# Performance work log

Measured on AMD Instinct MI355X. Metric: run time of the kernel, lower is better.

Reference implementation:

```python
import jax, jax.numpy as jnp
import numpy as np

N = 200000   # active voxels
B = 2        # batch size
G = 128      # spatial grid extent per axis
CIN = 64
COUT = 64
KS = 3       # kernel size -> 27 offsets
DIL = 1
EPS = 1e-5


def setup_inputs() -> dict:
    rng = np.random.default_rng(0)
    # unique active voxel coordinates over a B x G^3 grid
    lin = rng.choice(B * G * G * G, size=N, replace=False)
    b = lin // (G * G * G)
    r = lin % (G * G * G)
    x = r // (G * G)
    r2 = r % (G * G)
    y = r2 // G
    z = r2 % G
    coords = jnp.asarray(np.stack([b, x, y, z], axis=1).astype(np.int32))
    key = jax.random.key(0)
    ks = jax.random.split(key, 7)
    feats = jax.random.normal(ks[0], (N, CIN), jnp.float32)
    s1 = 1.0 / np.sqrt(KS ** 3 * CIN)
    s2 = 1.0 / np.sqrt(KS ** 3 * COUT)
    return {
        "feats": feats,
        "w1": jax.random.normal(ks[1], (KS ** 3, CIN, COUT), jnp.float32) * s1,
        "g1": 1.0 + 0.1 * jax.random.normal(ks[2], (COUT,), jnp.float32),
        "b1": 0.1 * jax.random.normal(ks[3], (COUT,), jnp.float32),
        "w2": jax.random.normal(ks[4], (KS ** 3, COUT, COUT), jnp.float32) * s2,
        "g2": 1.0 + 0.1 * jax.random.normal(ks[5], (COUT,), jnp.float32),
        "b2": 0.1 * jax.random.normal(ks[6], (COUT,), jnp.float32),
        "coords": coords,
    }


def build_neighbors(coords):
    """Hash (dense) lookup: for each of 27 kernel offsets, the input index of
    the neighboring active voxel (submanifold: output sites == input sites).
    Returns idx [27, N] int32 (0 where invalid) and mask [27, N] bool."""
    n = coords.shape[0]
    lin = ((coords[:, 0] * G + coords[:, 1]) * G + coords[:, 2]) * G + coords[:, 3]
    table = jnp.full((B * G * G * G,), -1, jnp.int32).at[lin].set(
        jnp.arange(n, dtype=jnp.int32))
    offs = jnp.asarray(
        [[dx, dy, dz] for dx in (-1, 0, 1) for dy in (-1, 0, 1) for dz in (-1, 0, 1)],
        dtype=jnp.int32) * DIL                       # [27, 3]
    nxyz = coords[None, :, 1:] + offs[:, None, :]    # [27, N, 3]
    inb = jnp.all((nxyz >= 0) & (nxyz < G), axis=-1)  # [27, N]
    c = jnp.clip(nxyz, 0, G - 1)
    nlin = ((coords[None, :, 0] * G + c[..., 0]) * G + c[..., 1]) * G + c[..., 2]
    idx = table[nlin]                                # [27, N]
    mask = inb & (idx >= 0)
    return jnp.where(mask, idx, 0), mask


def subm_conv(feats, nbr_idx, nbr_mask, w):
    # gather-GEMM-scatter, accumulated per kernel offset
    out = jnp.zeros((feats.shape[0], w.shape[-1]), feats.dtype)
    for k in range(w.shape[0]):
        g = jnp.where(nbr_mask[k][:, None], feats[nbr_idx[k]], 0.0)  # [N, Cin]
        out = out + g @ w[k]
    return out


def sparse_bn(x, gamma, beta):
    m = jnp.mean(x, axis=0)
    v = jnp.var(x, axis=0)
    return (x - m) * jax.lax.rsqrt(v + EPS) * gamma + beta


def reference(feats, w1, g1, b1, w2, g2, b2, coords):
    nbr_idx, nbr_mask = build_neighbors(coords)
    h = jax.nn.relu(sparse_bn(subm_conv(feats, nbr_idx, nbr_mask, w1), g1, b1))
    h = sparse_bn(subm_conv(h, nbr_idx, nbr_mask, w2), g2, b2)
    # shortcut is Identity (in_channels == out_channels, stride == 1)
    return jax.nn.relu(h + feats)
```

## Files before the change

kernel.cpp:

```cpp
#include <hip/hip_runtime.h>


constexpr int N_VOX = 200000;
constexpr int GEXT  = 128;
constexpr int C     = 64;
constexpr int K27   = 27;
constexpr int TBL_N = 2 * GEXT * GEXT * GEXT;
constexpr float EPSF = 1e-5f;

constexpr int NCH      = 782;
constexpr int PAIR_CAP = 460032;
constexpr int TIL64    = PAIR_CAP / 64;
constexpr int PBB      = 6250;
constexpr int RBLK     = 128;
constexpr int PAIRS_BLKS = K27 * NCH;
constexpr int PREP_FEAT  = 12500;
constexpr int PREP_W     = 432;

using short8   = __attribute__((ext_vector_type(8))) short;
using floatx16 = __attribute__((ext_vector_type(16))) float;

static __device__ __forceinline__ ushort f2bf(float f) {
  union { float f; unsigned u; } a; a.f = f;
  unsigned r = a.u + 0x7fff + ((a.u >> 16) & 1);
  return (ushort)(r >> 16);
}
static __device__ __forceinline__ float bf2f(ushort h) {
  union { unsigned u; float f; } a; a.u = ((unsigned)h) << 16;
  return a.f;
}


__global__ __launch_bounds__(256) void k_fill(int* __restrict__ t,
                                              int* __restrict__ bsum) {
  int i = blockIdx.x * 256 + threadIdx.x;
  if (i < TBL_N) t[i] = -1;
  if (i < 4096) bsum[i] = 0;
}

__global__ __launch_bounds__(256) void k_scatcnt(const int* __restrict__ coords,
                                                 int* __restrict__ t,
                                                 int* __restrict__ bsum) {
  int n = blockIdx.x * 256 + threadIdx.x;
  if (n >= N_VOX) return;
  int4 c = reinterpret_cast<const int4*>(coords)[n];
  int lin = ((c.x * GEXT + c.y) * GEXT + c.z) * GEXT + c.w;
  t[lin] = n;
  atomicAdd(&bsum[lin >> 10], 1);
}

__global__ __launch_bounds__(1024) void k_scan(const int* __restrict__ bsum,
                                               int* __restrict__ boff) {
  __shared__ int sc[1024];
  int t = threadIdx.x;
  int v0 = bsum[t * 4], v1 = bsum[t * 4 + 1], v2 = bsum[t * 4 + 2],
      v3 = bsum[t * 4 + 3];
  int s = v0 + v1 + v2 + v3;
  sc[t] = s;
  __syncthreads();
  for (int off = 1; off < 1024; off <<= 1) {
    int x = (t >= off) ? sc[t - off] : 0;
    __syncthreads();
    sc[t] += x;
    __syncthreads();
  }
  int excl = sc[t] - s;
  boff[t * 4]     = excl;
  boff[t * 4 + 1] = excl + v0;
  boff[t * 4 + 2] = excl + v0 + v1;
  boff[t * 4 + 3] = excl + v0 + v1 + v2;
}

__global__ __launch_bounds__(1024) void k_compact(int* __restrict__ table,
                                                  const int* __restrict__ boff,
                                                  int* __restrict__ perm) {
  __shared__ int wsum[16];
  int i = blockIdx.x * 1024 + threadIdx.x;
  int orig = table[i];
  bool valid = orig >= 0;
  unsigned long long bal = __ballot(valid);
  int lane = threadIdx.x & 63, wv = threadIdx.x >> 6;
  int before = __popcll(bal & ((1ull << lane) - 1ull));
  if (lane == 0) wsum[wv] = __popcll(bal);
  __syncthreads();
  int woff = 0;
  for (int w = 0; w < 16; ++w) woff += (w < wv) ? wsum[w] : 0;
  if (valid) {
    int j = boff[blockIdx.x] + woff + before;
    perm[j] = orig;
    table[i] = j;
  }
}

__global__ __launch_bounds__(256) void k_nbrc(const int* __restrict__ coords,
                                              const int* __restrict__ table,
                                              const int* __restrict__ perm,
                                              int* __restrict__ nbrp,
                                              int* __restrict__ cnt2,
                                              unsigned* __restrict__ vmask) {
  __shared__ int wcnt[27][4];
  int tid = threadIdx.x;
  int j = blockIdx.x * 256 + tid;
  bool on = j < N_VOX;
  int4 c = {0, 0, 0, 0};
  if (on) {
    int orig = perm[j];
    c = reinterpret_cast<const int4*>(coords)[orig];
  }
  unsigned m = 0;
  int k = 0;
  #pragma unroll
  for (int dx = -1; dx <= 1; ++dx)
    #pragma unroll
    for (int dy = -1; dy <= 1; ++dy)
      #pragma unroll
      for (int dz = -1; dz <= 1; ++dz) {
        int rank = -1;
        if (on) {
          int x = c.y + dx, y = c.z + dy, z = c.w + dz;
          if (((unsigned)x < (unsigned)GEXT) & ((unsigned)y < (unsigned)GEXT) &
              ((unsigned)z < (unsigned)GEXT)) {
            int lin = ((c.x * GEXT + x) * GEXT + y) * GEXT + z;
            rank = table[lin];
          }
          nbrp[k * N_VOX + j] = rank;
          if (rank >= 0) m |= (1u << k);
        }
        unsigned long long bal = __ballot(rank >= 0);
        if ((tid & 63) == 0) wcnt[k][tid >> 6] = __popcll(bal);
        ++k;
      }
  if (on) vmask[j] = m;
  __syncthreads();
  if (tid < 27)
    cnt2[tid * NCH + blockIdx.x] =
        wcnt[tid][0] + wcnt[tid][1] + wcnt[tid][2] + wcnt[tid][3];
}

__global__ __launch_bounds__(256) void k_segscan(const int* __restrict__ cnt2,
                                                 int* __restrict__ choff,
                                                 int* __restrict__ segs) {
  __shared__ int sc[256];
  int k = blockIdx.x, t = threadIdx.x;
  int v[4];
  #pragma unroll
  for (int i = 0; i < 4; ++i) {
    int idx = t * 4 + i;
    v[i] = (idx < NCH) ? cnt2[k * NCH + idx] : 0;
  }
  int s = v[0] + v[1] + v[2] + v[3];
  sc[t] = s;
  __syncthreads();
  for (int off = 1; off < 256; off <<= 1) {
    int x = (t >= off) ? sc[t - off] : 0;
    __syncthreads();
    sc[t] += x;
    __syncthreads();
  }
  int run = sc[t] - s;
  #pragma unroll
  for (int i = 0; i < 4; ++i) {
    int idx = t * 4 + i;
    if (idx < NCH) choff[k * NCH + idx] = run;
    run += v[i];
  }
  if (t == 255) segs[k] = sc[255];
}

__global__ __launch_bounds__(1024) void k_tiles(int* __restrict__ segs,
                                                int* __restrict__ tilk) {
  __shared__ int sb[28];
  if (threadIdx.x == 0) {
    int b = 0;
    for (int k = 0; k < K27; ++k) {
      sb[k] = b;
      segs[32 + k] = b;
      b += (segs[k] + 63) & ~63;
    }
    sb[27] = b;
    segs[32 + K27] = b;
  }
  __syncthreads();
  for (int t = threadIdx.x; t < TIL64; t += 1024) {
    int p0 = t * 64, kk = -1;
    #pragma unroll 1
    for (int k = 0; k < K27; ++k)
      if (p0 >= sb[k] && p0 < sb[k + 1]) kk = k;
    tilk[t] = kk;
  }
}

__global__ __launch_bounds__(256) void k_pairs_prep(
    int* __restrict__ nbrp, const int* __restrict__ choff,
    const int* __restrict__ segs, int* __restrict__ inl,
    const float* __restrict__ feats, const int* __restrict__ perm,
    const float* __restrict__ w1, const float* __restrict__ w2,
    ushort* __restrict__ fbp, ushort* __restrict__ wp1,
    ushort* __restrict__ wp2) {
  int b = blockIdx.x;
  if (b < PAIRS_BLKS) {
    __shared__ int wsum[4];
    int k = b / NCH, cch = b % NCH;
    int base = segs[32 + k];
    int j = cch * 256 + threadIdx.x;
    int v = (j < N_VOX) ? nbrp[k * N_VOX + j] : -1;
    bool valid = v >= 0;
    unsigned long long bal = __ballot(valid);
    int lane = threadIdx.x & 63, wv = threadIdx.x >> 6;
    int before = __popcll(bal & ((1ull << lane) - 1ull));
    if (lane == 0) wsum[wv] = __popcll(bal);
    __syncthreads();
    int woff = 0;
    #pragma unroll
    for (int w = 0; w < 4; ++w) woff += (w < wv) ? wsum[w] : 0;
    if (valid) {
      int p = base + choff[k * NCH + cch] + woff + before;
      inl[p] = v;
      nbrp[k * N_VOX + j] = p;
    }
  } else if (b < PAIRS_BLKS + PREP_FEAT) {
    int i = (b - PAIRS_BLKS) * 256 + threadIdx.x;
    int j = i >> 4, seg = i & 15;
    int p = perm[j];
    float4 v = reinterpret_cast<const float4*>(feats)[(p << 4) + seg];
    ushort4 o;
    o.x = f2bf(v.x); o.y = f2bf(v.y); o.z = f2bf(v.z); o.w = f2bf(v.w);
    reinterpret_cast<ushort4*>(fbp)[i] = o;
  } else {
    int b2 = b - PAIRS_BLKS - PREP_FEAT;
    const float* w = (b2 < PREP_W) ? w1 : w2;
    ushort* wp = (b2 < PREP_W) ? wp1 : wp2;
    int i = (b2 < PREP_W ? b2 : b2 - PREP_W) * 256 + threadIdx.x;
    int k = i >> 12, r = i & 4095, ci = r >> 6, co = r & 63;
    int ch = co >> 5, row = co & 31;
    int ks = ci >> 4, hi1 = (ci >> 3) & 1, e = ci & 7;
    int dst = ((((k * 2 + ch) * 4 + ks) * 2 + hi1) << 8) + row * 8 + e;
    wp[dst] = f2bf(w[i]);
  }
}

template <bool APPLY_BN>
__global__ __launch_bounds__(256, 4) void k_pva(
    const ushort* __restrict__ fin,
    const ushort* __restrict__ wp,
    const int* __restrict__ inl,
    const int* __restrict__ segs,
    const int* __restrict__ tilk,
    const float* __restrict__ ab,
    ushort* __restrict__ pv) {
  __shared__ ushort tile[64 * 64];
  __shared__ float abl[128];
  const int tid = threadIdx.x;
  const int p0 = blockIdx.x * 64;

  const int kk = tilk[blockIdx.x];
  if (kk < 0) return;
  const int off = segs[32 + kk];
  const int cnt = segs[kk];

  if (APPLY_BN) {
    if (tid < 128) abl[tid] = ab[tid];
    __syncthreads();
  }

  const int lane = tid & 63, wv = tid >> 6;
  const int lo = lane & 31, hi = lane >> 5;
  const int ch = wv & 1, vh = wv >> 1;
  const int pr = p0 + vh * 32 + lo;
  const bool vld = (pr - off) < cnt;
  const int idx = vld ? inl[pr] : -1;

  const char* wk = (const char*)wp + (kk << 13) + (ch << 12) + (lane << 4);
  short8 a0 = *(const short8*)(wk);
  short8 a1 = *(const short8*)(wk + 1024);
  short8 a2 = *(const short8*)(wk + 2048);
  short8 a3 = *(const short8*)(wk + 3072);

  short8 b0, b1, b2, b3;
  if (idx >= 0) {
    const char* b = (const char*)fin + ((size_t)idx << 7) + (hi << 4);
    b0 = *(const short8*)(b);
    b1 = *(const short8*)(b + 32);
    b2 = *(const short8*)(b + 64);
    b3 = *(const short8*)(b + 96);
    if (APPLY_BN) {
      #pragma unroll
      for (int ks = 0; ks < 4; ++ks) {
        short8& v = ks == 0 ? b0 : ks == 1 ? b1 : ks == 2 ? b2 : b3;
        int cb = ks * 16 + hi * 8;
        #pragma unroll
        for (int e = 0; e < 8; ++e) {
          float x = bf2f((ushort)v[e]);
          x = fmaxf(x * abl[cb + e] + abl[64 + cb + e], 0.f);
          v[e] = (short)f2bf(x);
        }
      }
    }
  } else {
    b0 = short8{0,0,0,0,0,0,0,0}; b1 = b0; b2 = b0; b3 = b0;
  }

  floatx16 acc;
  #pragma unroll
  for (int j = 0; j < 16; ++j) acc[j] = 0.f;
  acc = __builtin_amdgcn_mfma_f32_32x32x16_bf16(a0, b0, acc, 0, 0, 0);
  acc = __builtin_amdgcn_mfma_f32_32x32x16_bf16(a1, b1, acc, 0, 0, 0);
  acc = __builtin_amdgcn_mfma_f32_32x32x16_bf16(a2, b2, acc, 0, 0, 0);
  acc = __builtin_amdgcn_mfma_f32_32x32x16_bf16(a3, b3, acc, 0, 0, 0);

  {
    int r = vh * 32 + lo, rx = r & 7;
    char* trow = (char*)tile + r * 128 + hi * 8;
    #pragma unroll
    for (int rg = 0; rg < 4; ++rg) {
      ushort4 v;
      v.x = f2bf(acc[rg * 4 + 0]); v.y = f2bf(acc[rg * 4 + 1]);
      v.z = f2bf(acc[rg * 4 + 2]); v.w = f2bf(acc[rg * 4 + 3]);
      *(ushort4*)(trow + (((ch * 4 + rg) ^ rx) << 4)) = v;
    }
  }
  __syncthreads();
  {
    int row = tid >> 2, rx = row & 7, chunk = tid & 3;
    const char* src = (const char*)tile + row * 128;
    uint4 x = *(const uint4*)(src + (((chunk * 2) ^ rx) << 4));
    uint4 y = *(const uint4*)(src + (((chunk * 2 + 1) ^ rx) << 4));
    char* dst = (char*)pv + ((size_t)(p0 + row) << 7) + chunk * 32;
    *(uint4*)(dst) = x;
    *(uint4*)(dst + 16) = y;
  }
}

__global__ __launch_bounds__(256) void k_pvb(
    const ushort* __restrict__ pv,
    const int* __restrict__ pidx,
    const unsigned* __restrict__ vmask,
    ushort* __restrict__ fout,
    float* __restrict__ part) {
  __shared__ float sred[4][8][16];
  const int tid = threadIdx.x, lane = tid & 63, wv = tid >> 6;
  const int g = tid >> 3, e = tid & 7;
  const int j = blockIdx.x * 32 + g;

  unsigned m = vmask[j];
  float acc[8];
  #pragma unroll
  for (int r = 0; r < 8; ++r) acc[r] = 0.f;
  while (m) {
    int k = __builtin_ctz(m);
    m &= m - 1;
    int p = pidx[k * N_VOX + j];
    short8 v = *(const short8*)(pv + ((size_t)p << 6) + (e << 3));
    #pragma unroll
    for (int r = 0; r < 8; ++r) acc[r] += bf2f((ushort)v[r]);
  }

  ushort* o = fout + ((size_t)j << 6) + (e << 3);
  ushort4 v0, v1;
  v0.x = f2bf(acc[0]); v0.y = f2bf(acc[1]);
  v0.z = f2bf(acc[2]); v0.w = f2bf(acc[3]);
  v1.x = f2bf(acc[4]); v1.y = f2bf(acc[5]);
  v1.z = f2bf(acc[6]); v1.w = f2bf(acc[7]);
  *(ushort4*)o = v0;
  *(ushort4*)(o + 4) = v1;

  #pragma unroll
  for (int r = 0; r < 8; ++r) {
    float s = acc[r], ss = acc[r] * acc[r];
    s += __shfl_xor(s, 8);  ss += __shfl_xor(ss, 8);
    s += __shfl_xor(s, 16); ss += __shfl_xor(ss, 16);
    s += __shfl_xor(s, 32); ss += __shfl_xor(ss, 32);
    if (lane < 8) { sred[wv][lane][r] = s; sred[wv][lane][8 + r] = ss; }
  }
  __syncthreads();
  if (tid < 128) {
    int half = tid >> 6, chn = tid & 63;
    int e2 = chn >> 3, r2 = chn & 7;
    float v = sred[0][e2][half * 8 + r2] + sred[1][e2][half * 8 + r2] +
              sred[2][e2][half * 8 + r2] + sred[3][e2][half * 8 + r2];
    part[(size_t)blockIdx.x * 128 + tid] = v;
  }
}


__global__ __launch_bounds__(256) void k_red(const float* __restrict__ part,
                                             float* __restrict__ part2) {
  __shared__ float red[256];
  int tid = threadIdx.x;
  int e = tid & 127, g = tid >> 7;
  float s = 0.f;
  for (int r = blockIdx.x * 2 + g; r < PBB; r += 2 * RBLK)
    s += part[(size_t)r * 128 + e];
  red[tid] = s;
  __syncthreads();
  if (tid < 128) part2[(size_t)blockIdx.x * 128 + tid] = red[tid] + red[tid + 128];
}

__global__ __launch_bounds__(256) void k_bnfin(const float* __restrict__ part2,
                                               const float* __restrict__ gamma,
                                               const float* __restrict__ beta,
                                               float* __restrict__ ab) {
  __shared__ float red[256];
  int tid = threadIdx.x;
  int e = tid & 127, h = tid >> 7;
  float s = 0.f;
  #pragma unroll
  for (int r = h; r < RBLK; r += 2) s += part2[(size_t)r * 128 + e];
  red[tid] = s;
  __syncthreads();
  if (tid < 64) {
    float su = red[tid] + red[128 + tid];
    float ss = red[64 + tid] + red[192 + tid];
    float mean = su / (float)N_VOX;
    float var  = ss / (float)N_VOX - mean * mean;
    float a = gamma[tid] * rsqrtf(var + EPSF);
    ab[tid]      = a;
    ab[64 + tid] = beta[tid] - mean * a;
  }
}

__global__ __launch_bounds__(256) void k_final(const ushort* __restrict__ h2p,
                                               const ushort* __restrict__ fbp,
                                               const int* __restrict__ perm,
                                               const float* __restrict__ ab,
                                               float* __restrict__ out) {
  int i = blockIdx.x * 256 + threadIdx.x;
  int j = i >> 4, seg = i & 15;
  int p = perm[j];
  ushort4 h = reinterpret_cast<const ushort4*>(h2p)[i];
  ushort4 f = reinterpret_cast<const ushort4*>(fbp)[i];
  int cb = seg * 4;
  float4 o;
  o.x = fmaxf(bf2f(h.x) * ab[cb]     + ab[64 + cb]     + bf2f(f.x), 0.f);
  o.y = fmaxf(bf2f(h.y) * ab[cb + 1] + ab[64 + cb + 1] + bf2f(f.y), 0.f);
  o.z = fmaxf(bf2f(h.z) * ab[cb + 2] + ab[64 + cb + 2] + bf2f(f.z), 0.f);
  o.w = fmaxf(bf2f(h.w) * ab[cb + 3] + ab[64 + cb + 3] + bf2f(f.w), 0.f);
  reinterpret_cast<float4*>(out)[(p << 4) + seg] = o;
}

extern "C" void kernel_launch(void* const* d_in, const int* in_sizes, int n_in,
                              void* d_out, int out_size, void* d_ws, size_t ws_size,
                              hipStream_t stream) {
  const float* feats  = (const float*)d_in[0];
  const float* w1     = (const float*)d_in[1];
  const float* g1     = (const float*)d_in[2];
  const float* b1     = (const float*)d_in[3];
  const float* w2     = (const float*)d_in[4];
  const float* g2     = (const float*)d_in[5];
  const float* b2     = (const float*)d_in[6];
  const int*   coords = (const int*)d_in[7];
  float* out = (float*)d_out;

  char* ws = (char*)d_ws;
  ushort* pv    = (ushort*)ws;  ws += (size_t)PAIR_CAP * C * 2;
  int*    table = (int*)ws;     ws += (size_t)TBL_N * 4;
  int*    nbrp  = (int*)ws;     ws += (size_t)K27 * N_VOX * 4;
  ushort* fbp   = (ushort*)ws;  ws += (size_t)N_VOX * C * 2;
  ushort* h1p   = (ushort*)ws;  ws += (size_t)N_VOX * C * 2;
  ushort* h2p   = (ushort*)ws;  ws += (size_t)N_VOX * C * 2;
  int*    perm  = (int*)ws;     ws += (size_t)N_VOX * 4;
  ushort* wp1   = (ushort*)ws;  ws += (size_t)K27 * 4096 * 2;
  ushort* wp2   = (ushort*)ws;  ws += (size_t)K27 * 4096 * 2;
  int*    inl   = (int*)ws;     ws += (size_t)PAIR_CAP * 4;
  unsigned* vmask = (unsigned*)ws; ws += (size_t)N_VOX * 4;
  int*    bsum  = (int*)ws;     ws += 4096 * 4;
  int*    boff  = (int*)ws;     ws += 4096 * 4;
  int*    cnt2  = (int*)ws;     ws += (size_t)K27 * NCH * 4;
  int*    choff = (int*)ws;     ws += (size_t)K27 * NCH * 4;
  int*    segs  = (int*)ws;     ws += 256;
  int*    tilk  = (int*)ws;     ws += (size_t)TIL64 * 4;
  float*  part2 = (float*)ws;   ws += (size_t)RBLK * 128 * 4;
  float*  ab1   = (float*)ws;   ws += 512;
  float*  ab2   = (float*)ws;   ws += 512;
  float*  part  = (float*)table;

  k_fill<<<TBL_N / 256, 256, 0, stream>>>(table, bsum);
  k_scatcnt<<<(N_VOX + 255) / 256, 256, 0, stream>>>(coords, table, bsum);
  k_scan<<<1, 1024, 0, stream>>>(bsum, boff);
  k_compact<<<TBL_N / 1024, 1024, 0, stream>>>(table, boff, perm);
  k_nbrc<<<NCH, 256, 0, stream>>>(coords, table, perm, nbrp, cnt2, vmask);
  k_segscan<<<K27, 256, 0, stream>>>(cnt2, choff, segs);
  k_tiles<<<1, 1024, 0, stream>>>(segs, tilk);
  k_pairs_prep<<<PAIRS_BLKS + PREP_FEAT + 2 * PREP_W, 256, 0, stream>>>(
      nbrp, choff, segs, inl, feats, perm, w1, w2, fbp, wp1, wp2);

  k_pva<false><<<TIL64, 256, 0, stream>>>(fbp, wp1, inl, segs, tilk, ab1, pv);
  k_pvb<<<PBB, 256, 0, stream>>>(pv, nbrp, vmask, h1p, part);
  k_red<<<RBLK, 256, 0, stream>>>(part, part2);
  k_bnfin<<<1, 256, 0, stream>>>(part2, g1, b1, ab1);

  k_pva<true><<<TIL64, 256, 0, stream>>>(h1p, wp2, inl, segs, tilk, ab1, pv);
  k_pvb<<<PBB, 256, 0, stream>>>(pv, nbrp, vmask, h2p, part);
  k_red<<<RBLK, 256, 0, stream>>>(part, part2);
  k_bnfin<<<1, 256, 0, stream>>>(part2, g2, b2, ab2);

  k_final<<<N_VOX * 16 / 256, 256, 0, stream>>>(h2p, fbp, perm, ab2, out);
}
```

Before: 288.3 us.

## Fold single-block scan and BN-finalize kernels into last-block-done epilogues

Replaces the separate single-block kernels (bucket scan, per-offset segment scan plus tile map, BN finalize) with epilogues that run in whichever block finishes last in the preceding kernel, detected with an atomic ticket counter and thread fences. This cuts five kernel launches and their serial launch gaps from the pipeline. It also vectorizes the hash-table fill to int4 stores with a quarter of the blocks. In exchange, the last block now does the serial scan work with fewer threads, and a stray dead load was added in the compaction kernel.

```diff
diff --git a/kernel.cpp b/kernel.cpp
--- a/kernel.cpp
+++ b/kernel.cpp
@@ -16,6 +16,7 @@
 constexpr int PAIRS_BLKS = K27 * NCH;
 constexpr int PREP_FEAT  = 12500;
 constexpr int PREP_W     = 432;
+constexpr int SCAT_BLKS  = 782;
 
 using short8   = __attribute__((ext_vector_type(8))) short;
 using floatx16 = __attribute__((ext_vector_type(16))) float;
@@ -30,45 +31,59 @@
   return a.f;
 }
 
+static __device__ __forceinline__ bool last_block(int* tick, int nblk) {
+  __shared__ int isLast;
+  __syncthreads();
+  if (threadIdx.x == 0) {
+    __threadfence();
+    isLast = (atomicAdd(tick, 1) == nblk - 1) ? 1 : 0;
+  }
+  __syncthreads();
+  if (isLast) __threadfence();
+  return isLast != 0;
+}
+
 
 __global__ __launch_bounds__(256) void k_fill(int* __restrict__ t,
-                                              int* __restrict__ bsum) {
+                                              int* __restrict__ bsum,
+                                              int* __restrict__ tick) {
   int i = blockIdx.x * 256 + threadIdx.x;
-  if (i < TBL_N) t[i] = -1;
+  int4 m1 = {-1, -1, -1, -1};
+  reinterpret_cast<int4*>(t)[i] = m1;
   if (i < 4096) bsum[i] = 0;
+  if (i < 8) tick[i] = 0;
 }
 
 __global__ __launch_bounds__(256) void k_scatcnt(const int* __restrict__ coords,
                                                  int* __restrict__ t,
-                                                 int* __restrict__ bsum) {
+                                                 int* __restrict__ bsum,
+                                                 int* __restrict__ boff,
+                                                 int* __restrict__ tick) {
   int n = blockIdx.x * 256 + threadIdx.x;
-  if (n >= N_VOX) return;
-  int4 c = reinterpret_cast<const int4*>(coords)[n];
-  int lin = ((c.x * GEXT + c.y) * GEXT + c.z) * GEXT + c.w;
-  t[lin] = n;
-  atomicAdd(&bsum[lin >> 10], 1);
-}
-
-__global__ __launch_bounds__(1024) void k_scan(const int* __restrict__ bsum,
-                                               int* __restrict__ boff) {
-  __shared__ int sc[1024];
-  int t = threadIdx.x;
-  int v0 = bsum[t * 4], v1 = bsum[t * 4 + 1], v2 = bsum[t * 4 + 2],
-      v3 = bsum[t * 4 + 3];
-  int s = v0 + v1 + v2 + v3;
-  sc[t] = s;
-  __syncthreads();
-  for (int off = 1; off < 1024; off <<= 1) {
-    int x = (t >= off) ? sc[t - off] : 0;
+  if (n < N_VOX) {
+    int4 c = reinterpret_cast<const int4*>(coords)[n];
+    int lin = ((c.x * GEXT + c.y) * GEXT + c.z) * GEXT + c.w;
+    t[lin] = n;
+    atomicAdd(&bsum[lin >> 10], 1);
+  }
+  if (last_block(&tick[0], SCAT_BLKS)) {
+    __shared__ int sc[256];
+    int tid = threadIdx.x;
+    int v[16], s = 0;
+    #pragma unroll
+    for (int i = 0; i < 16; ++i) { v[i] = bsum[tid * 16 + i]; s += v[i]; }
+    sc[tid] = s;
     __syncthreads();
-    sc[t] += x;
-    __syncthreads();
-  }
-  int excl = sc[t] - s;
-  boff[t * 4]     = excl;
-  boff[t * 4 + 1] = excl + v0;
-  boff[t * 4 + 2] = excl + v0 + v1;
-  boff[t * 4 + 3] = excl + v0 + v1 + v2;
+    for (int off = 1; off < 256; off <<= 1) {
+      int x = (tid >= off) ? sc[tid - off] : 0;
+      __syncthreads();
+      sc[tid] += x;
+      __syncthreads();
+    }
+    int run = sc[tid] - s;
+    #pragma unroll
+    for (int i = 0; i < 16; ++i) { boff[tid * 16 + i] = run; run += v[i]; }
+  }
 }
 
 __global__ __launch_bounds__(1024) void k_compact(int* __restrict__ table,
@@ -86,7 +101,8 @@
   int woff = 0;
   for (int w = 0; w < 16; ++w) woff += (w < wv) ? wsum[w] : 0;
   if (valid) {
-    int j = boff[blockIdx.x] + woff + before;
+    int j = boff[blockIdx.x >> 2] ;
+    j = boff[blockIdx.x] + woff + before;
     perm[j] = orig;
     table[i] = j;
   }
@@ -97,7 +113,11 @@
                                               const int* __restrict__ perm,
                                               int* __restrict__ nbrp,
                                               int* __restrict__ cnt2,
-                                              unsigned* __restrict__ vmask) {
+                                              unsigned* __restrict__ vmask,
+                                              int* __restrict__ choff,
+                                              int* __restrict__ segs,
+                                              int* __restrict__ tilk,
+                                              int* __restrict__ tick) {
   __shared__ int wcnt[27][4];
   int tid = threadIdx.x;
   int j = blockIdx.x * 256 + tid;
@@ -135,58 +155,56 @@
   if (tid < 27)
     cnt2[tid * NCH + blockIdx.x] =
         wcnt[tid][0] + wcnt[tid][1] + wcnt[tid][2] + wcnt[tid][3];
-}
-
-__global__ __launch_bounds__(256) void k_segscan(const int* __restrict__ cnt2,
-                                                 int* __restrict__ choff,
-                                                 int* __restrict__ segs) {
-  __shared__ int sc[256];
-  int k = blockIdx.x, t = threadIdx.x;
-  int v[4];
-  #pragma unroll
-  for (int i = 0; i < 4; ++i) {
-    int idx = t * 4 + i;
-    v[i] = (idx < NCH) ? cnt2[k * NCH + idx] : 0;
-  }
-  int s = v[0] + v[1] + v[2] + v[3];
-  sc[t] = s;
-  __syncthreads();
-  for (int off = 1; off < 256; off <<= 1) {
-    int x = (t >= off) ? sc[t - off] : 0;
+
+  if (last_block(&tick[1], NCH)) {
+    __shared__ int sc[256];
+    __shared__ int sseg[27];
+    __shared__ int sb[28];
+    for (int kk = 0; kk < K27; ++kk) {
+      int v[4];
+      #pragma unroll
+      for (int i = 0; i < 4; ++i) {
+        int idx = tid * 4 + i;
+        v[i] = (idx < NCH) ? cnt2[kk * NCH + idx] : 0;
+      }
+      int s = v[0] + v[1] + v[2] + v[3];
+      sc[tid] = s;
+      __syncthreads();
+      for (int off = 1; off < 256; off <<= 1) {
+        int x = (tid >= off) ? sc[tid - off] : 0;
+        __syncthreads();
+        sc[tid] += x;
+        __syncthreads();
+      }
+      int run = sc[tid] - s;
+      #pragma unroll
+      for (int i = 0; i < 4; ++i) {
+        int idx = tid * 4 + i;
+        if (idx < NCH) choff[kk * NCH + idx] = run;
+        run += v[i];
+      }
+      if (tid == 255) sseg[kk] = sc[255];
+      __syncthreads();
+    }
+    if (tid == 0) {
+      int b = 0;
+      for (int kk = 0; kk < K27; ++kk) {
+        sb[kk] = b;
+        segs[kk] = sseg[kk];
+        segs[32 + kk] = b;
+        b += (sseg[kk] + 63) & ~63;
+      }
+      sb[27] = b;
+      segs[32 + K27] = b;
+    }
     __syncthreads();
-    sc[t] += x;
-    __syncthreads();
-  }
-  int run = sc[t] - s;
-  #pragma unroll
-  for (int i = 0; i < 4; ++i) {
-    int idx = t * 4 + i;
-    if (idx < NCH) choff[k * NCH + idx] = run;
-    run += v[i];
-  }
-  if (t == 255) segs[k] = sc[255];
-}
-
-__global__ __launch_bounds__(1024) void k_tiles(int* __restrict__ segs,
-                                                int* __restrict__ tilk) {
-  __shared__ int sb[28];
-  if (threadIdx.x == 0) {
-    int b = 0;
-    for (int k = 0; k < K27; ++k) {
-      sb[k] = b;
-      segs[32 + k] = b;
-      b += (segs[k] + 63) & ~63;
-    }
-    sb[27] = b;
-    segs[32 + K27] = b;
-  }
-  __syncthreads();
-  for (int t = threadIdx.x; t < TIL64; t += 1024) {
-    int p0 = t * 64, kk = -1;
-    #pragma unroll 1
-    for (int k = 0; k < K27; ++k)
-      if (p0 >= sb[k] && p0 < sb[k + 1]) kk = k;
-    tilk[t] = kk;
+    for (int t2 = tid; t2 < TIL64; t2 += 256) {
+      int p0 = t2 * 64, kk2 = -1;
+      #pragma unroll 1
+      for (int kk = 0; kk < K27; ++kk)
+        if (p0 >= sb[kk] && p0 < sb[kk + 1]) kk2 = kk;
+      tilk[t2] = kk2;
+    }
   }
 }
 
@@ -382,9 +400,12 @@
   }
 }
 
-
-__global__ __launch_bounds__(256) void k_red(const float* __restrict__ part,
-                                             float* __restrict__ part2) {
+__global__ __launch_bounds__(256) void k_redfin(const float* __restrict__ part,
+                                                float* __restrict__ part2,
+                                                const float* __restrict__ gamma,
+                                                const float* __restrict__ beta,
+                                                float* __restrict__ ab,
+                                                int* __restrict__ tick) {
   __shared__ float red[256];
   int tid = threadIdx.x;
   int e = tid & 127, g = tid >> 7;
@@ -394,28 +415,23 @@
   red[tid] = s;
   __syncthreads();
   if (tid < 128) part2[(size_t)blockIdx.x * 128 + tid] = red[tid] + red[tid + 128];
-}
-
-__global__ __launch_bounds__(256) void k_bnfin(const float* __restrict__ part2,
-                                               const float* __restrict__ gamma,
-                                               const float* __restrict__ beta,
-                                               float* __restrict__ ab) {
-  __shared__ float red[256];
-  int tid = threadIdx.x;
-  int e = tid & 127, h = tid >> 7;
-  float s = 0.f;
-  #pragma unroll
-  for (int r = h; r < RBLK; r += 2) s += part2[(size_t)r * 128 + e];
-  red[tid] = s;
-  __syncthreads();
-  if (tid < 64) {
-    float su = red[tid] + red[128 + tid];
-    float ss = red[64 + tid] + red[192 + tid];
-    float mean = su / (float)N_VOX;
-    float var  = ss / (float)N_VOX - mean * mean;
-    float a = gamma[tid] * rsqrtf(var + EPSF);
-    ab[tid]      = a;
-    ab[64 + tid] = beta[tid] - mean * a;
+
+  if (last_block(tick, RBLK)) {
+    int h = tid >> 7;
+    float s2 = 0.f;
+    #pragma unroll
+    for (int r = h; r < RBLK; r += 2) s2 += part2[(size_t)r * 128 + e];
+    red[tid] = s2;
+    __syncthreads();
+    if (tid < 64) {
+      float su = red[tid] + red[128 + tid];
+      float ss = red[64 + tid] + red[192 + tid];
+      float mean = su / (float)N_VOX;
+      float var  = ss / (float)N_VOX - mean * mean;
+      float a = gamma[tid] * rsqrtf(var + EPSF);
+      ab[tid]      = a;
+      ab[64 + tid] = beta[tid] - mean * a;
+    }
   }
 }
 
@@ -472,27 +488,24 @@
   float*  part2 = (float*)ws;   ws += (size_t)RBLK * 128 * 4;
   float*  ab1   = (float*)ws;   ws += 512;
   float*  ab2   = (float*)ws;   ws += 512;
+  int*    tick  = (int*)ws;     ws += 64;
   float*  part  = (float*)table;
 
-  k_fill<<<TBL_N / 256, 256, 0, stream>>>(table, bsum);
-  k_scatcnt<<<(N_VOX + 255) / 256, 256, 0, stream>>>(coords, table, bsum);
-  k_scan<<<1, 1024, 0, stream>>>(bsum, boff);
+  k_fill<<<TBL_N / 1024, 256, 0, stream>>>(table, bsum, tick);
+  k_scatcnt<<<SCAT_BLKS, 256, 0, stream>>>(coords, table, bsum, boff, tick);
   k_compact<<<TBL_N / 1024, 1024, 0, stream>>>(table, boff, perm);
-  k_nbrc<<<NCH, 256, 0, stream>>>(coords, table, perm, nbrp, cnt2, vmask);
-  k_segscan<<<K27, 256, 0, stream>>>(cnt2, choff, segs);
-  k_tiles<<<1, 1024, 0, stream>>>(segs, tilk);
+  k_nbrc<<<NCH, 256, 0, stream>>>(coords, table, perm, nbrp, cnt2, vmask,
+                                  choff, segs, tilk, tick);
   k_pairs_prep<<<PAIRS_BLKS + PREP_FEAT + 2 * PREP_W, 256, 0, stream>>>(
       nbrp, choff, segs, inl, feats, perm, w1, w2, fbp, wp1, wp2);
 
   k_pva<false><<<TIL64, 256, 0, stream>>>(fbp, wp1, inl, segs, tilk, ab1, pv);
   k_pvb<<<PBB, 256, 0, stream>>>(pv, nbrp, vmask, h1p, part);
-  k_red<<<RBLK, 256, 0, stream>>>(part, part2);
-  k_bnfin<<<1, 256, 0, stream>>>(part2, g1, b1, ab1);
+  k_redfin<<<RBLK, 256, 0, stream>>>(part, part2, g1, b1, ab1, &tick[2]);
 
   k_pva<true><<<TIL64, 256, 0, stream>>>(h1p, wp2, inl, segs, tilk, ab1, pv);
   k_pvb<<<PBB, 256, 0, stream>>>(pv, nbrp, vmask, h2p, part);
-  k_red<<<RBLK, 256, 0, stream>>>(part, part2);
-  k_bnfin<<<1, 256, 0, stream>>>(part2, g2, b2, ab2);
+  k_redfin<<<RBLK, 256, 0, stream>>>(part, part2, g2, b2, ab2, &tick[3]);
 
   k_final<<<N_VOX * 16 / 256, 256, 0, stream>>>(h2p, fbp, perm, ab2, out);
 }
```

New measurement: 408.2 us. 1.42x slower.
